# Kernel optimization log

Measured on AMD Instinct MI355X. Metric: run time of the kernel, lower is better.

The kernel has to match this reference:

```python
import jax, jax.numpy as jnp
import numpy as np

E = 256          # embedding_dim
IN = E + 1       # input feature dim (embedding_dim + 1)
B = 128          # batch
N = 1027         # nodes: 1 source + 1024 candidates + 1 destination + 1 depot
REWIRE_P = 0.1


def setup_inputs() -> dict:
    key = jax.random.key(0)
    ks = jax.random.split(key, 16)
    scale = 1.0 / np.sqrt(IN)

    def lin_w(k):
        return jax.random.normal(k, (E, IN), dtype=jnp.float32) * scale

    def lin_b(k):
        return jax.random.normal(k, (E,), dtype=jnp.float32) * scale

    # sparse small-world rewiring weights: nc scalar writes -> one scatter
    nc = int(IN * E * REWIRE_P)  # 6579
    rows = jax.random.randint(ks[10], (nc,), 0, E)
    cols = jax.random.randint(ks[11], (nc,), 0, IN)
    vals = jax.random.normal(ks[12], (nc,), dtype=jnp.float32) * 0.01
    W_rand = jnp.zeros((E, IN), dtype=jnp.float32).at[rows, cols].set(vals)

    return {
        "solutions": jax.random.normal(ks[0], (B, N, IN), dtype=jnp.float32),
        "W_src": lin_w(ks[1]), "b_src": lin_b(ks[2]),
        "W_dst": lin_w(ks[3]), "b_dst": lin_b(ks[4]),
        "W_dep": lin_w(ks[5]), "b_dep": lin_b(ks[6]),
        "W_cand": lin_w(ks[7]), "b_cand": lin_b(ks[8]),
        "W_reg": lin_w(ks[9]), "b_reg": lin_b(ks[13]),
        "W_rand": W_rand,
        "integration_weight": jnp.float32(0.3),
    }


def reference(solutions, W_src, b_src, W_dst, b_dst, W_dep, b_dep,
              W_cand, b_cand, W_reg, b_reg, W_rand, integration_weight):
    # slice node groups: [B,1,IN], [B,N-3,IN], [B,1,IN], [B,1,IN]
    src = solutions[:, :1, :]
    cand = solutions[:, 1:-2, :]
    dst = solutions[:, -2:-1, :]
    dep = solutions[:, -1:, :]

    def lin(x, W, b):
        return jnp.einsum('bnd,ed->bne', x, W) + b

    def sw(x):
        # SmallWorldLayer: regular linear + 0.1 * sparse random matmul
        return lin(x, W_reg, b_reg) + 0.1 * jnp.einsum('bnd,ed->bne', x, W_rand)

    alpha = jax.nn.sigmoid(integration_weight)

    def mix(emb, sw_out):
        return (1.0 - alpha) * emb + alpha * sw_out

    source_emb = mix(lin(src, W_src, b_src), sw(src))
    candidates_emb = mix(lin(cand, W_cand, b_cand), sw(cand))
    destination_emb = mix(lin(dst, W_dst, b_dst), sw(dst))
    depot_emb = mix(lin(dep, W_dep, b_dep), sw(dep))
    return (source_emb, candidates_emb, destination_emb, depot_emb)
```

## Files before the change

### kernel.cpp

```cpp
#include <hip/hip_runtime.h>
#include <hip/hip_bf16.h>

typedef __bf16 bf16x8 __attribute__((ext_vector_type(8)));
typedef float  f32x4  __attribute__((ext_vector_type(4)));

#define BATCH 128
#define NSOL  1027
#define IND   257
#define EMB   256
#define OUT_SRC  0ULL
#define OUT_CAND 32768ULL
#define OUT_DST  33587200ULL
#define OUT_DEP  33619968ULL

#define WFRAG_OFF 0
#define BEFF_OFF  147456
#define WT_OFF    151552

__device__ __forceinline__ void gload_lds16(const void* g, void* l) {
    __builtin_amdgcn_global_load_lds((const __attribute__((address_space(1))) void*)g,
                                     (__attribute__((address_space(3))) void*)l,
                                     16, 0, 0);
}

__global__ __launch_bounds__(256) void swne_prep(
    const float* __restrict__ Wsrc, const float* __restrict__ bsrc,
    const float* __restrict__ Wdst, const float* __restrict__ bdst,
    const float* __restrict__ Wdep, const float* __restrict__ bdep,
    const float* __restrict__ Wcand, const float* __restrict__ bcand,
    const float* __restrict__ Wreg, const float* __restrict__ breg,
    const float* __restrict__ Wrand, const float* __restrict__ iw,
    char* __restrict__ ws)
{
    const float a  = 1.0f / (1.0f + expf(-iw[0]));
    const float ca = 1.0f - a;
    const float sa = 0.1f * a;

    const float* Ws[4] = {Wsrc, Wcand, Wdst, Wdep};
    const float* Bs[4] = {bsrc, bcand, bdst, bdep};

    const int gid = blockIdx.x * 256 + threadIdx.x;
    const int gsz = gridDim.x * 256;

    float* beff = (float*)(ws + BEFF_OFF);
    for (int i = gid; i < 4 * EMB; i += gsz) {
        int seg = i >> 8, e = i & 255;
        beff[i] = ca * Bs[seg][e] + a * breg[e];
    }

    float* wt = (float*)(ws + WT_OFF);
    for (int i = gid; i < 4 * IND * EMB; i += gsz) {
        int seg = i / (IND * EMB);
        int rem = i - seg * (IND * EMB);
        int k = rem >> 8, e = rem & 255;
        int si = e * IND + k;
        wt[i] = ca * Ws[seg][si] + a * Wreg[si] + sa * Wrand[si];
    }

    __bf16* wfr = (__bf16*)(ws + WFRAG_OFF);
    for (int i = gid; i < 9 * 16 * 64 * 8; i += gsz) {
        int kk   = i >> 13;
        int rem  = i & 8191;
        int ntg  = rem >> 9;
        int rem2 = rem & 511;
        int l    = rem2 >> 3;
        int j    = rem2 & 7;
        int e = ntg * 16 + (l & 15);
        int k = kk * 32 + (l >> 4) * 8 + j;
        float v = 0.0f;
        if (k < IND) {
            int si = e * IND + k;
            v = ca * Wcand[si] + a * Wreg[si] + sa * Wrand[si];
        }
        wfr[i] = (__bf16)v;
    }
}

__global__ __launch_bounds__(256) void swne_main(const float* __restrict__ sol,
                                                 const char* __restrict__ ws,
                                                 float* __restrict__ out)
{
    __shared__ float lds_a[8448];
    const int tid = threadIdx.x;
    const int bid = blockIdx.x;
    const float* beff = (const float*)(ws + BEFF_OFF);

    if (bid < 384) {
        int s = bid >> 7;
        int b = bid & 127;
        int nrow  = (s == 0) ? 0 : (s == 1 ? 1025 : 1026);
        int segw  = (s == 0) ? 0 : (s == 1 ? 2 : 3);
        size_t outb = (s == 0) ? OUT_SRC : (s == 1 ? OUT_DST : OUT_DEP);
        const float* x = sol + (size_t)(b * NSOL + nrow) * IND;
        for (int i = tid; i < IND; i += 256) lds_a[i] = x[i];
        __syncthreads();
        const float* wtp = (const float*)(ws + WT_OFF) + (size_t)segw * (IND * EMB) + tid;
        float s0 = 0.f, s1 = 0.f, s2 = 0.f, s3 = 0.f;
        #pragma unroll 4
        for (int k = 0; k < 256; k += 4) {
            s0 = fmaf(lds_a[k + 0], wtp[(size_t)(k + 0) * 256], s0);
            s1 = fmaf(lds_a[k + 1], wtp[(size_t)(k + 1) * 256], s1);
            s2 = fmaf(lds_a[k + 2], wtp[(size_t)(k + 2) * 256], s2);
            s3 = fmaf(lds_a[k + 3], wtp[(size_t)(k + 3) * 256], s3);
        }
        float sum = beff[segw * 256 + tid] + ((s0 + s1) + (s2 + s3))
                  + lds_a[256] * wtp[(size_t)256 * 256];
        out[outb + (size_t)b * 256 + tid] = sum;
        return;
    }

    const int cbid = bid - 384;
    const int bb = cbid >> 5;
    const int t  = cbid & 31;
    const size_t base_byte = (size_t)(bb * NSOL + 1 + t * 32) * IND * 4;
    const size_t S0 = base_byte & ~(size_t)15;
    const int h = (int)((base_byte - S0) >> 2);

    const int lane = tid & 63, wave = tid >> 6;

    for (int c = wave; c < 33; c += 4)
        gload_lds16((const char*)sol + S0 + (size_t)c * 1024 + (size_t)lane * 16,
                    (char*)lds_a + c * 1024);
    __syncthreads();

    f32x4 acc[2][4];
    #pragma unroll
    for (int rt = 0; rt < 2; ++rt)
        #pragma unroll
        for (int nt = 0; nt < 4; ++nt) {
            f32x4 z = {0.f, 0.f, 0.f, 0.f};
            acc[rt][nt] = z;
        }

    const int rl = lane & 15, grp = lane >> 4;
    const bf16x8* wf8 = (const bf16x8*)(ws + WFRAG_OFF);
    const int ntb = wave * 4;

    #pragma unroll
    for (int kk = 0; kk < 9; ++kk) {
        bf16x8 af[2];
        #pragma unroll
        for (int rt = 0; rt < 2; ++rt) {
            const float* ap = &lds_a[h + (rt * 16 + rl) * IND + kk * 32 + grp * 8];
            bf16x8 v;
            #pragma unroll
            for (int j = 0; j < 8; ++j) v[j] = (__bf16)ap[j];
            af[rt] = v;
        }
        #pragma unroll
        for (int nt = 0; nt < 4; ++nt) {
            bf16x8 bv = wf8[(size_t)(kk * 16 + ntb + nt) * 64 + lane];
            #pragma unroll
            for (int rt = 0; rt < 2; ++rt)
                acc[rt][nt] = __builtin_amdgcn_mfma_f32_16x16x32_bf16(af[rt], bv, acc[rt][nt], 0, 0, 0);
        }
    }

    float bvals[4];
    #pragma unroll
    for (int nt = 0; nt < 4; ++nt)
        bvals[nt] = beff[256 + wave * 64 + nt * 16 + rl];

    float* outc = out + OUT_CAND + (size_t)(bb * 1024 + t * 32) * 256 + wave * 64 + rl;
    #pragma unroll
    for (int rt = 0; rt < 2; ++rt)
        #pragma unroll
        for (int nt = 0; nt < 4; ++nt)
            #pragma unroll
            for (int i = 0; i < 4; ++i) {
                int row = rt * 16 + grp * 4 + i;
                outc[(size_t)row * 256 + nt * 16] = acc[rt][nt][i] + bvals[nt];
            }
}

extern "C" void kernel_launch(void* const* d_in, const int* in_sizes, int n_in,
                              void* d_out, int out_size, void* d_ws, size_t ws_size,
                              hipStream_t stream) {
    const float* sol   = (const float*)d_in[0];
    const float* Wsrc  = (const float*)d_in[1];
    const float* bsrc  = (const float*)d_in[2];
    const float* Wdst  = (const float*)d_in[3];
    const float* bdst  = (const float*)d_in[4];
    const float* Wdep  = (const float*)d_in[5];
    const float* bdep  = (const float*)d_in[6];
    const float* Wcand = (const float*)d_in[7];
    const float* bcand = (const float*)d_in[8];
    const float* Wreg  = (const float*)d_in[9];
    const float* breg  = (const float*)d_in[10];
    const float* Wrand = (const float*)d_in[11];
    const float* iw    = (const float*)d_in[12];

    swne_prep<<<512, 256, 0, stream>>>(Wsrc, bsrc, Wdst, bdst, Wdep, bdep,
                                       Wcand, bcand, Wreg, breg, Wrand, iw,
                                       (char*)d_ws);
    swne_main<<<4480, 256, 0, stream>>>(sol, (const char*)d_ws, (float*)d_out);
}
```

Measured before the change: 71.24 us.

## Load candidate rows directly from global and vectorize output stores via swapped MFMA

The candidate GEMM path no longer stages the 32-row input tile in 33 KB of LDS through global_load_lds. Each lane now reads its own row slice straight from global memory with unaligned float4 loads. The MFMA operands are swapped so each lane holds four consecutive output columns, which lets it write float4 vector stores instead of scalar strided stores. The much smaller LDS footprint and the added launch-bounds occupancy hint aim to fit more blocks per CU. The cost is that input loads are now uncoalesced per-lane reads with no shared staging, and they run past the 257-wide row into zero-weighted padding.

After: 129.9 us. 82.3% more time.

```diff
diff --git a/kernel.cpp b/kernel.cpp
--- a/kernel.cpp
+++ b/kernel.cpp
@@ -3,6 +3,7 @@
 
 typedef __bf16 bf16x8 __attribute__((ext_vector_type(8)));
 typedef float  f32x4  __attribute__((ext_vector_type(4)));
+typedef float  f32x4u __attribute__((ext_vector_type(4), aligned(4)));
 
 #define BATCH 128
 #define NSOL  1027
@@ -16,12 +17,6 @@
 #define WFRAG_OFF 0
 #define BEFF_OFF  147456
 #define WT_OFF    151552
-
-__device__ __forceinline__ void gload_lds16(const void* g, void* l) {
-    __builtin_amdgcn_global_load_lds((const __attribute__((address_space(1))) void*)g,
-                                     (__attribute__((address_space(3))) void*)l,
-                                     16, 0, 0);
-}
 
 __global__ __launch_bounds__(256) void swne_prep(
     const float* __restrict__ Wsrc, const float* __restrict__ bsrc,
@@ -76,11 +71,11 @@
     }
 }
 
-__global__ __launch_bounds__(256) void swne_main(const float* __restrict__ sol,
-                                                 const char* __restrict__ ws,
-                                                 float* __restrict__ out)
+__global__ __launch_bounds__(256, 4) void swne_main(const float* __restrict__ sol,
+                                                    const char* __restrict__ ws,
+                                                    float* __restrict__ out)
 {
-    __shared__ float lds_a[8448];
+    __shared__ float xrow[260];
     const int tid = threadIdx.x;
     const int bid = blockIdx.x;
     const float* beff = (const float*)(ws + BEFF_OFF);
@@ -92,19 +87,19 @@
         int segw  = (s == 0) ? 0 : (s == 1 ? 2 : 3);
         size_t outb = (s == 0) ? OUT_SRC : (s == 1 ? OUT_DST : OUT_DEP);
         const float* x = sol + (size_t)(b * NSOL + nrow) * IND;
-        for (int i = tid; i < IND; i += 256) lds_a[i] = x[i];
+        for (int i = tid; i < IND; i += 256) xrow[i] = x[i];
         __syncthreads();
         const float* wtp = (const float*)(ws + WT_OFF) + (size_t)segw * (IND * EMB) + tid;
         float s0 = 0.f, s1 = 0.f, s2 = 0.f, s3 = 0.f;
         #pragma unroll 4
         for (int k = 0; k < 256; k += 4) {
-            s0 = fmaf(lds_a[k + 0], wtp[(size_t)(k + 0) * 256], s0);
-            s1 = fmaf(lds_a[k + 1], wtp[(size_t)(k + 1) * 256], s1);
-            s2 = fmaf(lds_a[k + 2], wtp[(size_t)(k + 2) * 256], s2);
-            s3 = fmaf(lds_a[k + 3], wtp[(size_t)(k + 3) * 256], s3);
+            s0 = fmaf(xrow[k + 0], wtp[(size_t)(k + 0) * 256], s0);
+            s1 = fmaf(xrow[k + 1], wtp[(size_t)(k + 1) * 256], s1);
+            s2 = fmaf(xrow[k + 2], wtp[(size_t)(k + 2) * 256], s2);
+            s3 = fmaf(xrow[k + 3], wtp[(size_t)(k + 3) * 256], s3);
         }
         float sum = beff[segw * 256 + tid] + ((s0 + s1) + (s2 + s3))
-                  + lds_a[256] * wtp[(size_t)256 * 256];
+                  + xrow[256] * wtp[(size_t)256 * 256];
         out[outb + (size_t)b * 256 + tid] = sum;
         return;
     }
@@ -112,16 +107,12 @@
     const int cbid = bid - 384;
     const int bb = cbid >> 5;
     const int t  = cbid & 31;
-    const size_t base_byte = (size_t)(bb * NSOL + 1 + t * 32) * IND * 4;
-    const size_t S0 = base_byte & ~(size_t)15;
-    const int h = (int)((base_byte - S0) >> 2);
 
     const int lane = tid & 63, wave = tid >> 6;
+    const int rl = lane & 15, grp = lane >> 4;
 
-    for (int c = wave; c < 33; c += 4)
-        gload_lds16((const char*)sol + S0 + (size_t)c * 1024 + (size_t)lane * 16,
-                    (char*)lds_a + c * 1024);
-    __syncthreads();
+    const float* arow0 = sol + (size_t)(bb * NSOL + 1 + t * 32 + rl) * IND;
+    const float* arow1 = arow0 + (size_t)16 * IND;
 
     f32x4 acc[2][4];
     #pragma unroll
@@ -132,19 +123,21 @@
             acc[rt][nt] = z;
         }
 
-    const int rl = lane & 15, grp = lane >> 4;
     const bf16x8* wf8 = (const bf16x8*)(ws + WFRAG_OFF);
     const int ntb = wave * 4;
 
     #pragma unroll
     for (int kk = 0; kk < 9; ++kk) {
+        const int k0 = kk * 32 + grp * 8;
         bf16x8 af[2];
         #pragma unroll
         for (int rt = 0; rt < 2; ++rt) {
-            const float* ap = &lds_a[h + (rt * 16 + rl) * IND + kk * 32 + grp * 8];
+            const float* ap = (rt == 0 ? arow0 : arow1) + k0;
+            f32x4 lo = *(const f32x4u*)(ap);
+            f32x4 hi = *(const f32x4u*)(ap + 4);
             bf16x8 v;
             #pragma unroll
-            for (int j = 0; j < 8; ++j) v[j] = (__bf16)ap[j];
+            for (int j = 0; j < 4; ++j) { v[j] = (__bf16)lo[j]; v[j + 4] = (__bf16)hi[j]; }
             af[rt] = v;
         }
         #pragma unroll
@@ -152,25 +145,22 @@
             bf16x8 bv = wf8[(size_t)(kk * 16 + ntb + nt) * 64 + lane];
             #pragma unroll
             for (int rt = 0; rt < 2; ++rt)
-                acc[rt][nt] = __builtin_amdgcn_mfma_f32_16x16x32_bf16(af[rt], bv, acc[rt][nt], 0, 0, 0);
+                acc[rt][nt] = __builtin_amdgcn_mfma_f32_16x16x32_bf16(bv, af[rt], acc[rt][nt], 0, 0, 0);
         }
     }
 
-    float bvals[4];
+    const float* bc = beff + 256;
     #pragma unroll
-    for (int nt = 0; nt < 4; ++nt)
-        bvals[nt] = beff[256 + wave * 64 + nt * 16 + rl];
-
-    float* outc = out + OUT_CAND + (size_t)(bb * 1024 + t * 32) * 256 + wave * 64 + rl;
-    #pragma unroll
-    for (int rt = 0; rt < 2; ++rt)
+    for (int rt = 0; rt < 2; ++rt) {
+        const size_t mrow = (size_t)(bb * 1024 + t * 32 + rt * 16 + rl);
+        float* op = out + OUT_CAND + mrow * 256 + wave * 64 + grp * 4;
         #pragma unroll
-        for (int nt = 0; nt < 4; ++nt)
-            #pragma unroll
-            for (int i = 0; i < 4; ++i) {
-                int row = rt * 16 + grp * 4 + i;
-                outc[(size_t)row * 256 + nt * 16] = acc[rt][nt][i] + bvals[nt];
-            }
+        for (int nt = 0; nt < 4; ++nt) {
+            f32x4 bv4 = *(const f32x4*)(bc + wave * 64 + nt * 16 + grp * 4);
+            f32x4 r = acc[rt][nt] + bv4;
+            *(f32x4*)(op + nt * 16) = r;
+        }
+    }
 }
 
 extern "C" void kernel_launch(void* const* d_in, const int* in_sizes, int n_in,
```
